# Kernel optimization log

Hardware: AMD Instinct MI355X
Metric: run time of the kernel (lower is better)

Reference implementation:

```python
import jax, jax.numpy as jnp
import numpy as np


def setup_inputs() -> dict:
    key = jax.random.key(0)
    kq, kk, kv = jax.random.split(key, 3)
    B, Q, K, D = 8, 2048, 2048, 1024
    return {
        "queries": jax.random.normal(kq, (B, Q, D), dtype=jnp.float32),
        "keys": jax.random.normal(kk, (B, K, D), dtype=jnp.float32),
        "values": jax.random.normal(kv, (B, K, D), dtype=jnp.float32),
    }


def reference(queries, keys, values):
    # scores: [B, Q, K] = queries @ keys^T
    scores = jnp.einsum("bqd,bkd->bqk", queries, keys)
    # NOTE: softmax over dim=1, i.e. the QUERY axis (non-standard)
    attn = jax.nn.softmax(scores, axis=1)
    # output: [B, Q, D]
    return jnp.einsum("bqk,bkd->bqd", attn, values)
```

## Files before the change

kernel.cpp:

```cpp
#include <hip/hip_runtime.h>
#include <stdint.h>

typedef _Float16 half8 __attribute__((ext_vector_type(8)));
typedef __attribute__((ext_vector_type(4))) float f32x4;
typedef __attribute__((ext_vector_type(8))) unsigned short us8;

__device__ inline unsigned short f2h(float x) {
  _Float16 h = (_Float16)x;
  return __builtin_bit_cast(unsigned short, h);
}

__device__ inline void ld16(const unsigned short* g, unsigned short* l) {
  __builtin_amdgcn_global_load_lds(
      (const __attribute__((address_space(1))) unsigned int*)g,
      (__attribute__((address_space(3))) unsigned int*)l, 16, 0, 0);
}

__global__ void k_cast16(const float* __restrict__ in, unsigned short* __restrict__ o, long n8) {
  long i = (long)blockIdx.x * blockDim.x + threadIdx.x;
  if (i >= n8) return;
  float4 a = ((const float4*)in)[i * 2];
  float4 b = ((const float4*)in)[i * 2 + 1];
  us8 h;
  h[0] = f2h(a.x); h[1] = f2h(a.y); h[2] = f2h(a.z); h[3] = f2h(a.w);
  h[4] = f2h(b.x); h[5] = f2h(b.y); h[6] = f2h(b.z); h[7] = f2h(b.w);
  *(us8*)(o + i * 8) = h;
}

__global__ void k_transpose16(const float* __restrict__ V, unsigned short* __restrict__ VT,
                              int Kn, int Dn) {
  __shared__ unsigned short t[64][65];
  const int b = blockIdx.z;
  const int k0 = blockIdx.x * 64, d0 = blockIdx.y * 64;
  const int c = threadIdx.x & 63, rr = threadIdx.x >> 6;
  const float* pV = V + (long)b * Kn * Dn;
  unsigned short* pT = VT + (long)b * Dn * Kn;
#pragma unroll
  for (int i = 0; i < 16; ++i) {
    int r = rr + i * 4;
    t[r][c] = f2h(pV[(long)(k0 + r) * Dn + d0 + c]);
  }
  __syncthreads();
#pragma unroll
  for (int i = 0; i < 16; ++i) {
    int r = rr + i * 4;
    pT[(long)(d0 + r) * Kn + k0 + c] = t[c][r];
  }
}


#define SBAR() __builtin_amdgcn_s_barrier()
#define SCHED0() __builtin_amdgcn_sched_barrier(0)
#define LGKM0() do { asm volatile("s_waitcnt lgkmcnt(0)" ::: "memory"); SCHED0(); } while (0)
#define VMC(n) do { asm volatile("s_waitcnt vmcnt(" #n ")" ::: "memory"); } while (0)

template <int STATS>
__launch_bounds__(512, 2)
__global__ void k_gemm_bt(const unsigned short* __restrict__ A,
                          const unsigned short* __restrict__ B,
                          float* __restrict__ C, float2* __restrict__ ps,
                          int N, int Kin, long sA, long sB, long sC) {
  __shared__ unsigned short sAb[4][256 * 32];
  __shared__ unsigned short sBb[4][256 * 32];

  const int tid = threadIdx.x;
  const int lane = tid & 63, wave = tid >> 6;
  const int wr = wave >> 2, wc = wave & 3;
  const int l15 = lane & 15;

  const int nx = gridDim.x, ny = gridDim.y;
  int wg = ((int)blockIdx.z * ny + blockIdx.y) * nx + blockIdx.x;
  const int nwg = nx * ny * (int)gridDim.z;
  wg = (wg & 7) * (nwg >> 3) + (wg >> 3);
  const int tn = wg % nx, tm = (wg / nx) % ny, b = wg / (nx * ny);

  const unsigned short* pA = A + b * sA + (long)tm * 256 * Kin;
  const unsigned short* pB = B + b * sB + (long)tn * 256 * Kin;
  float* pC = C + b * sC;

  const int rlo = tid >> 2;
  const int csw = ((tid & 3) * 8) ^ (((rlo >> 1) & 3) << 3);
  const long ga = (long)rlo * Kin + csw;
  const long gh = (long)128 * Kin;

  const int ksw = ((lane >> 4) * 8) ^ (((l15 >> 1) & 3) << 3);
  const int aoff = (wr * 128 + l15) * 32 + ksw;
  const int boff = (wc * 64 + l15) * 32 + ksw;

#define STG_A(t, q) do { \
    ld16(pA + ga + (long)(t) * 32, &sAb[q][tid * 8]); \
    ld16(pA + ga + gh + (long)(t) * 32, &sAb[q][4096 + tid * 8]); } while (0)
#define STG_B(t, q) do { \
    ld16(pB + ga + (long)(t) * 32, &sBb[q][tid * 8]); \
    ld16(pB + ga + gh + (long)(t) * 32, &sBb[q][4096 + tid * 8]); } while (0)

#define LDA8(q, m) (*(const half8*)&sAb[q][aoff + (m) * 512])
#define LDB8(q, n) (*(const half8*)&sBb[q][boff + (n) * 512])

  f32x4 acc[8][4];
#pragma unroll
  for (int i = 0; i < 8; ++i)
#pragma unroll
    for (int j = 0; j < 4; ++j)
#pragma unroll
      for (int r = 0; r < 4; ++r) acc[i][j][r] = 0.f;

  half8 fa0, fa1, fa2, fa3, fb0, fb1, fb2, fb3;

#define MFMA4(m, a) \
  acc[m][0] = __builtin_amdgcn_mfma_f32_16x16x32_f16(a, fb0, acc[m][0], 0, 0, 0); \
  acc[m][1] = __builtin_amdgcn_mfma_f32_16x16x32_f16(a, fb1, acc[m][1], 0, 0, 0); \
  acc[m][2] = __builtin_amdgcn_mfma_f32_16x16x32_f16(a, fb2, acc[m][2], 0, 0, 0); \
  acc[m][3] = __builtin_amdgcn_mfma_f32_16x16x32_f16(a, fb3, acc[m][3], 0, 0, 0);

#define PH_READ_AB(q) \
  fa0 = LDA8(q, 0); fa1 = LDA8(q, 1); fa2 = LDA8(q, 2); fa3 = LDA8(q, 3); \
  fb0 = LDB8(q, 0); fb1 = LDB8(q, 1); fb2 = LDB8(q, 2); fb3 = LDB8(q, 3);

#define PH_READ_A(q) \
  fa0 = LDA8(q, 4); fa1 = LDA8(q, 5); fa2 = LDA8(q, 6); fa3 = LDA8(q, 7);

#define PH_MFMA_LO \
  __builtin_amdgcn_s_setprio(1); \
  MFMA4(0, fa0) MFMA4(1, fa1) MFMA4(2, fa2) MFMA4(3, fa3) \
  __builtin_amdgcn_s_setprio(0);

#define PH_MFMA_HI \
  __builtin_amdgcn_s_setprio(1); \
  MFMA4(4, fa0) MFMA4(5, fa1) MFMA4(6, fa2) MFMA4(7, fa3) \
  __builtin_amdgcn_s_setprio(0);

  const int nt = Kin >> 5;
  const int ni = nt >> 1;

  STG_A(0, 0); STG_B(0, 0);
  STG_A(1, 1); STG_B(1, 1);
  VMC(4); SCHED0(); SBAR();

  for (int it = 0; it + 1 < ni; ++it) {
    const int t0 = it * 2;
    const int q0 = t0 & 3, q1 = q0 + 1;
    const int r0 = q0 ^ 2, r1 = q1 ^ 2;
    PH_READ_AB(q0)
    STG_A(t0 + 2, r0);
    SCHED0(); SBAR(); LGKM0();
    PH_MFMA_LO
    SCHED0(); SBAR();
    PH_READ_A(q0)
    STG_B(t0 + 2, r0);
    SCHED0(); SBAR(); LGKM0();
    PH_MFMA_HI
    VMC(4); SCHED0(); SBAR();
    PH_READ_AB(q1)
    STG_A(t0 + 3, r1);
    SCHED0(); SBAR(); LGKM0();
    PH_MFMA_LO
    SCHED0(); SBAR();
    PH_READ_A(q1)
    STG_B(t0 + 3, r1);
    SCHED0(); SBAR(); LGKM0();
    PH_MFMA_HI
    VMC(4); SCHED0(); SBAR();
  }
  {
    const int q0 = (nt - 2) & 3, q1 = q0 + 1;
    PH_READ_AB(q0)
    SCHED0(); SBAR(); LGKM0();
    PH_MFMA_LO
    SCHED0(); SBAR();
    PH_READ_A(q0)
    SCHED0(); SBAR(); LGKM0();
    PH_MFMA_HI
    VMC(0); SCHED0(); SBAR();
    PH_READ_AB(q1)
    LGKM0();
    PH_MFMA_LO
    PH_READ_A(q1)
    LGKM0();
    PH_MFMA_HI
  }

  const int crow0 = tm * 256 + wr * 128 + (lane >> 4) * 4;
  const int ccol0 = tn * 256 + wc * 64 + l15;
#pragma unroll
  for (int m = 0; m < 8; ++m)
#pragma unroll
    for (int n = 0; n < 4; ++n)
#pragma unroll
      for (int r = 0; r < 4; ++r)
        pC[(long)(crow0 + m * 16 + r) * N + ccol0 + n * 16] = acc[m][n][r];

  if constexpr (STATS) {
#pragma unroll
    for (int n = 0; n < 4; ++n) {
      float mx = -3.0e38f;
#pragma unroll
      for (int m = 0; m < 8; ++m)
#pragma unroll
        for (int r = 0; r < 4; ++r) mx = fmaxf(mx, acc[m][n][r]);
      mx = fmaxf(mx, __shfl_xor(mx, 16, 64));
      mx = fmaxf(mx, __shfl_xor(mx, 32, 64));
      float l = 0.f;
#pragma unroll
      for (int m = 0; m < 8; ++m)
#pragma unroll
        for (int r = 0; r < 4; ++r) l += __expf(acc[m][n][r] - mx);
      l += __shfl_xor(l, 16, 64);
      l += __shfl_xor(l, 32, 64);
      if (lane < 16) {
        int col = tn * 256 + wc * 64 + n * 16 + lane;
        ps[((long)(b * 16 + tm * 2 + wr)) * N + col] = make_float2(mx, l);
      }
    }
  }
}

__global__ void k_stats_combine(const float2* __restrict__ ps, float2* __restrict__ st, int Kn) {
  const long i = (long)blockIdx.x * blockDim.x + threadIdx.x;
  const int b = (int)(i / Kn), k = (int)(i % Kn);
  float M = -3.0e38f;
#pragma unroll
  for (int j = 0; j < 16; ++j) M = fmaxf(M, ps[((long)(b * 16 + j)) * Kn + k].x);
  float L = 0.f;
#pragma unroll
  for (int j = 0; j < 16; ++j) {
    float2 v = ps[((long)(b * 16 + j)) * Kn + k];
    L += v.y * __expf(v.x - M);
  }
  st[i] = make_float2(M, 1.0f / L);
}

__global__ void k_pcomp(const float* __restrict__ S, const float2* __restrict__ st,
                        unsigned short* __restrict__ P) {
  const long i = (long)blockIdx.x * blockDim.x + threadIdx.x;
  const long r = i >> 8;
  const int kb = (int)(i & 255) * 8;
  const int b = (int)(r >> 11);
  const float* sp = S + r * 2048 + kb;
  float4 s0 = *(const float4*)sp;
  float4 s1 = *(const float4*)(sp + 4);
  const float2* tp = st + (long)b * 2048 + kb;
  us8 o;
  float sv[8] = {s0.x, s0.y, s0.z, s0.w, s1.x, s1.y, s1.z, s1.w};
#pragma unroll
  for (int j = 0; j < 8; ++j) {
    float2 t = tp[j];
    o[j] = f2h(__expf(sv[j] - t.x) * t.y);
  }
  *(us8*)(P + r * 2048 + kb) = o;
}

extern "C" void kernel_launch(void* const* d_in, const int* in_sizes, int n_in,
                              void* d_out, int out_size, void* d_ws, size_t ws_size,
                              hipStream_t stream) {
  const float* Q = (const float*)d_in[0];
  const float* Kp = (const float*)d_in[1];
  const float* V = (const float*)d_in[2];
  float* out = (float*)d_out;

  constexpr int Bb = 8, Qn = 2048, Kn = 2048, Dn = 1024;
  constexpr long QD = (long)Qn * Dn, KD = (long)Kn * Dn, QK = (long)Qn * Kn, DK = (long)Dn * Kn;

  const size_t per = 3 * (size_t)(QD * 2)
                   + (size_t)(QK * 4)
                   + (size_t)(QK * 2)
                   + (size_t)(16 * Kn * 8)
                   + (size_t)(Kn * 8);
  int cb = 8;
  while (cb > 1 && (size_t)cb * per > ws_size) cb >>= 1;

  char* w = (char*)d_ws;
  unsigned short* q16 = (unsigned short*)w; w += (size_t)cb * QD * 2;
  unsigned short* k16 = (unsigned short*)w; w += (size_t)cb * KD * 2;
  unsigned short* vt  = (unsigned short*)w; w += (size_t)cb * DK * 2;
  float* S            = (float*)w;          w += (size_t)cb * QK * 4;
  unsigned short* P   = (unsigned short*)w; w += (size_t)cb * QK * 2;
  float2* ps          = (float2*)w;         w += (size_t)cb * 16 * Kn * 8;
  float2* st          = (float2*)w;

  for (int b0 = 0; b0 < Bb; b0 += cb) {
    int nb = (cb < Bb - b0) ? cb : (Bb - b0);
    long n8 = (long)nb * QD / 8;
    k_cast16<<<(int)(n8 / 256), 256, 0, stream>>>(Q + b0 * QD, q16, n8);
    k_cast16<<<(int)(n8 / 256), 256, 0, stream>>>(Kp + b0 * KD, k16, n8);
    k_transpose16<<<dim3(Kn / 64, Dn / 64, nb), 256, 0, stream>>>(V + b0 * KD, vt, Kn, Dn);
    k_gemm_bt<1><<<dim3(Kn / 256, Qn / 256, nb), 512, 0, stream>>>(
        q16, k16, S, ps, Kn, Dn, QD, KD, QK);
    k_stats_combine<<<nb * Kn / 256, 256, 0, stream>>>(ps, st, Kn);
    k_pcomp<<<(int)((long)nb * QK / 8 / 256), 256, 0, stream>>>(S, st, P);
    k_gemm_bt<0><<<dim3(Dn / 256, Qn / 256, nb), 512, 0, stream>>>(
        P, vt, out + b0 * QD, nullptr, Dn, Kn, QK, DK, QD);
  }
}
```

Baseline: 460.0 us.

## Software-pipeline LDS fragment reads with register double buffering and fewer barriers

Restructures the fp16 MFMA GEMM main loop so the next tile's low A and B fragments are read from LDS into a second register set while the current tile's high-half MFMAs run. The A and B global-to-LDS stages are merged into one staging step. Each tile now uses one barrier instead of four, and the explicit lgkmcnt(0) waits are dropped in favour of compiler-inserted waits. The aim is to cut barrier stalls and hide LDS latency behind MFMA work, at the cost of extra VGPRs for the doubled fragment buffers, which could add register pressure at 2 blocks per CU.

```diff
diff --git a/kernel.cpp b/kernel.cpp
--- a/kernel.cpp
+++ b/kernel.cpp
@@ -51,7 +51,6 @@
 
 #define SBAR() __builtin_amdgcn_s_barrier()
 #define SCHED0() __builtin_amdgcn_sched_barrier(0)
-#define LGKM0() do { asm volatile("s_waitcnt lgkmcnt(0)" ::: "memory"); SCHED0(); } while (0)
 #define VMC(n) do { asm volatile("s_waitcnt vmcnt(" #n ")" ::: "memory"); } while (0)
 
 template <int STATS>
@@ -87,10 +86,9 @@
   const int aoff = (wr * 128 + l15) * 32 + ksw;
   const int boff = (wc * 64 + l15) * 32 + ksw;
 
-#define STG_A(t, q) do { \
+#define STG(t, q) do { \
     ld16(pA + ga + (long)(t) * 32, &sAb[q][tid * 8]); \
-    ld16(pA + ga + gh + (long)(t) * 32, &sAb[q][4096 + tid * 8]); } while (0)
-#define STG_B(t, q) do { \
+    ld16(pA + ga + gh + (long)(t) * 32, &sAb[q][4096 + tid * 8]); \
     ld16(pB + ga + (long)(t) * 32, &sBb[q][tid * 8]); \
     ld16(pB + ga + gh + (long)(t) * 32, &sBb[q][4096 + tid * 8]); } while (0)
 
@@ -105,79 +103,61 @@
 #pragma unroll
       for (int r = 0; r < 4; ++r) acc[i][j][r] = 0.f;
 
-  half8 fa0, fa1, fa2, fa3, fb0, fb1, fb2, fb3;
-
-#define MFMA4(m, a) \
-  acc[m][0] = __builtin_amdgcn_mfma_f32_16x16x32_f16(a, fb0, acc[m][0], 0, 0, 0); \
-  acc[m][1] = __builtin_amdgcn_mfma_f32_16x16x32_f16(a, fb1, acc[m][1], 0, 0, 0); \
-  acc[m][2] = __builtin_amdgcn_mfma_f32_16x16x32_f16(a, fb2, acc[m][2], 0, 0, 0); \
-  acc[m][3] = __builtin_amdgcn_mfma_f32_16x16x32_f16(a, fb3, acc[m][3], 0, 0, 0);
-
-#define PH_READ_AB(q) \
-  fa0 = LDA8(q, 0); fa1 = LDA8(q, 1); fa2 = LDA8(q, 2); fa3 = LDA8(q, 3); \
-  fb0 = LDB8(q, 0); fb1 = LDB8(q, 1); fb2 = LDB8(q, 2); fb3 = LDB8(q, 3);
-
-#define PH_READ_A(q) \
-  fa0 = LDA8(q, 4); fa1 = LDA8(q, 5); fa2 = LDA8(q, 6); fa3 = LDA8(q, 7);
-
-#define PH_MFMA_LO \
+  half8 aL[2][4], bC[2][4], aH[4];
+
+#define READ_LO(s, q) \
+  aL[s][0] = LDA8(q, 0); aL[s][1] = LDA8(q, 1); aL[s][2] = LDA8(q, 2); aL[s][3] = LDA8(q, 3); \
+  bC[s][0] = LDB8(q, 0); bC[s][1] = LDB8(q, 1); bC[s][2] = LDB8(q, 2); bC[s][3] = LDB8(q, 3);
+
+#define READ_HI(q) \
+  aH[0] = LDA8(q, 4); aH[1] = LDA8(q, 5); aH[2] = LDA8(q, 6); aH[3] = LDA8(q, 7);
+
+#define MFMA_ROW(m, a, s) \
+  acc[m][0] = __builtin_amdgcn_mfma_f32_16x16x32_f16(a, bC[s][0], acc[m][0], 0, 0, 0); \
+  acc[m][1] = __builtin_amdgcn_mfma_f32_16x16x32_f16(a, bC[s][1], acc[m][1], 0, 0, 0); \
+  acc[m][2] = __builtin_amdgcn_mfma_f32_16x16x32_f16(a, bC[s][2], acc[m][2], 0, 0, 0); \
+  acc[m][3] = __builtin_amdgcn_mfma_f32_16x16x32_f16(a, bC[s][3], acc[m][3], 0, 0, 0);
+
+#define MFMA_LO(s) \
   __builtin_amdgcn_s_setprio(1); \
-  MFMA4(0, fa0) MFMA4(1, fa1) MFMA4(2, fa2) MFMA4(3, fa3) \
+  MFMA_ROW(0, aL[s][0], s) MFMA_ROW(1, aL[s][1], s) \
+  MFMA_ROW(2, aL[s][2], s) MFMA_ROW(3, aL[s][3], s) \
   __builtin_amdgcn_s_setprio(0);
 
-#define PH_MFMA_HI \
+#define MFMA_HI(s) \
   __builtin_amdgcn_s_setprio(1); \
-  MFMA4(4, fa0) MFMA4(5, fa1) MFMA4(6, fa2) MFMA4(7, fa3) \
+  MFMA_ROW(4, aH[0], s) MFMA_ROW(5, aH[1], s) \
+  MFMA_ROW(6, aH[2], s) MFMA_ROW(7, aH[3], s) \
   __builtin_amdgcn_s_setprio(0);
 
+#define TILE_MAIN(t, s, sn) \
+  READ_HI((t) & 3); \
+  STG((t) + 2, ((t) + 2) & 3); \
+  MFMA_LO(s) \
+  VMC(4); SBAR(); SCHED0(); \
+  READ_LO(sn, ((t) + 1) & 3); \
+  MFMA_HI(s)
+
   const int nt = Kin >> 5;
-  const int ni = nt >> 1;
-
-  STG_A(0, 0); STG_B(0, 0);
-  STG_A(1, 1); STG_B(1, 1);
-  VMC(4); SCHED0(); SBAR();
-
-  for (int it = 0; it + 1 < ni; ++it) {
-    const int t0 = it * 2;
-    const int q0 = t0 & 3, q1 = q0 + 1;
-    const int r0 = q0 ^ 2, r1 = q1 ^ 2;
-    PH_READ_AB(q0)
-    STG_A(t0 + 2, r0);
-    SCHED0(); SBAR(); LGKM0();
-    PH_MFMA_LO
-    SCHED0(); SBAR();
-    PH_READ_A(q0)
-    STG_B(t0 + 2, r0);
-    SCHED0(); SBAR(); LGKM0();
-    PH_MFMA_HI
-    VMC(4); SCHED0(); SBAR();
-    PH_READ_AB(q1)
-    STG_A(t0 + 3, r1);
-    SCHED0(); SBAR(); LGKM0();
-    PH_MFMA_LO
-    SCHED0(); SBAR();
-    PH_READ_A(q1)
-    STG_B(t0 + 3, r1);
-    SCHED0(); SBAR(); LGKM0();
-    PH_MFMA_HI
-    VMC(4); SCHED0(); SBAR();
+
+  STG(0, 0);
+  STG(1, 1);
+  VMC(4); SBAR(); SCHED0();
+  READ_LO(0, 0);
+
+  for (int t = 0; t + 3 < nt; t += 2) {
+    TILE_MAIN(t, 0, 1);
+    TILE_MAIN(t + 1, 1, 0);
   }
   {
-    const int q0 = (nt - 2) & 3, q1 = q0 + 1;
-    PH_READ_AB(q0)
-    SCHED0(); SBAR(); LGKM0();
-    PH_MFMA_LO
-    SCHED0(); SBAR();
-    PH_READ_A(q0)
-    SCHED0(); SBAR(); LGKM0();
-    PH_MFMA_HI
-    VMC(0); SCHED0(); SBAR();
-    PH_READ_AB(q1)
-    LGKM0();
-    PH_MFMA_LO
-    PH_READ_A(q1)
-    LGKM0();
-    PH_MFMA_HI
+    READ_HI((nt - 2) & 3);
+    MFMA_LO(0)
+    VMC(0); SBAR(); SCHED0();
+    READ_LO(1, (nt - 1) & 3);
+    MFMA_HI(0)
+    READ_HI((nt - 1) & 3);
+    MFMA_LO(1)
+    MFMA_HI(1)
   }
 
   const int crow0 = tm * 256 + wr * 128 + (lane >> 4) * 4;
```

Measured after the change: 411.5 us. -10.5%, faster.
